# Kernel tuning notes

Measured on AMD Instinct MI355X. Metric: run time of the kernel, lower is better.

Reference implementation:

```python
import jax, jax.numpy as jnp
import numpy as np

T, B, N, KALL, F, ORD, DIN, H, NH, HD, DE, DOUT = 4, 4, 16384, 4, 16384, 3, 4, 64, 4, 16, 4, 64


def setup_inputs() -> dict:
    key = jax.random.key(0)
    ks = jax.random.split(key, 32)
    p = lambda k, shape: (jax.random.normal(k, shape) * 0.1).astype(jnp.float32)
    indices = jax.random.randint(ks[0], (F, ORD), 0, N, dtype=jnp.int32)
    cnt = jnp.zeros((N,), jnp.float32).at[indices.reshape(-1)].add(1.0)
    nnz = jnp.maximum(cnt, 1.0)  # per-node nonzero count (avoid div-by-zero)
    return {
        "h": p(ks[1], (B, N, H)),
        "h_global": p(ks[2], (B, KALL, DOUT)),
        "x": p(ks[3], (T, B, N, DIN)),
        "extra": p(ks[4], (T, B, KALL, DE)),
        "dones": jax.random.bernoulli(ks[5], 0.1, (T, B)),
        "indices": indices,
        "nnz": nnz,
        # GRU cell params (flax GRUCell layout: i-dense with bias, h-dense no bias except n-gate)
        "Wi": p(ks[6], (DIN, 3 * H)), "bi": p(ks[7], (3 * H,)),
        "Wh": p(ks[8], (H, 3 * H)), "bhn": p(ks[9], (H,)),
        # MultiHeadAttention params
        "Wq": p(ks[10], (H, NH, HD)), "bq": p(ks[11], (NH, HD)),
        "Wk": p(ks[12], (H, NH, HD)), "bk": p(ks[13], (NH, HD)),
        "Wv": p(ks[14], (H, NH, HD)), "bv": p(ks[15], (NH, HD)),
        "Wo": p(ks[16], (NH, HD, H)), "bo": p(ks[17], (H,)),
        # output MLP (logit head) and value head
        "W1": p(ks[18], (H + DE, DOUT)), "b1": p(ks[19], (DOUT,)),
        "W2": p(ks[20], (DOUT, 1)), "b2": p(ks[21], (1,)),
        "Wv1": p(ks[22], (H + DE, 1)), "bv1": p(ks[23], (1,)),
    }


def reference(h, h_global, x, extra, dones, indices, nnz,
              Wi, bi, Wh, bhn, Wq, bq, Wk, bk, Wv, bv, Wo, bo,
              W1, b1, W2, b2, Wv1, bv1):
    Hd = Wh.shape[0]

    def gru_step(carry, inp):
        xt, dt = inp  # xt: [B,N,din], dt: [B]
        c = jnp.where(dt[:, None, None], jnp.zeros_like(carry), carry)
        gi = xt @ Wi + bi          # [B,N,3H]
        gh = c @ Wh                # [B,N,3H]
        r = jax.nn.sigmoid(gi[..., :Hd] + gh[..., :Hd])
        z = jax.nn.sigmoid(gi[..., Hd:2 * Hd] + gh[..., Hd:2 * Hd])
        n = jnp.tanh(gi[..., 2 * Hd:] + r * (gh[..., 2 * Hd:] + bhn))
        new = (1.0 - z) * n + z * c
        return new, new

    h_fin, hs = jax.lax.scan(gru_step, h, (x, dones))  # hs: [T,B,N,H]

    # gather per-factor neighbor hidden states
    g = jnp.take(hs, indices, axis=2)  # [T,B,F,ord,H]
    q = jnp.einsum('tbfkh,hnd->tbfknd', g, Wq) + bq
    kk = jnp.einsum('tbfkh,hnd->tbfknd', g, Wk) + bk
    vv = jnp.einsum('tbfkh,hnd->tbfknd', g, Wv) + bv
    scale = 1.0 / np.sqrt(q.shape[-1]).astype(np.float32)
    att = jax.nn.softmax(jnp.einsum('tbfqnd,tbfknd->tbfnqk', q * scale, kk), axis=-1)
    o = jnp.einsum('tbfnqk,tbfknd->tbfqnd', att, vv)
    a = jnp.einsum('tbfknd,ndh->tbfkh', o, Wo) + bo  # [T,B,F,ord,H]

    Tn, Bn = a.shape[0], a.shape[1]
    Nn = nnz.shape[0]
    a_flat = a.reshape(Tn, Bn, -1, a.shape[-1])  # [T,B,F*ord,H]
    # segment-sum scatter back to nodes, normalized by nnz
    y = jnp.zeros((Tn, Bn, Nn, a.shape[-1]), a.dtype).at[:, :, indices.reshape(-1), :].add(a_flat)
    y = y / nnz[None, None, :, None]

    Kall = extra.shape[2]
    N0 = Nn // Kall
    ypi = y.reshape(Tn, Bn, Kall, N0, y.shape[-1])
    y_global = jnp.mean(ypi, axis=3)                       # [T,B,K,H]
    z_global = jnp.concatenate((y_global, extra), axis=3)  # [T,B,K,H+DE]
    extra_t = jnp.broadcast_to(extra[:, :, :, None, :], (Tn, Bn, Kall, N0, extra.shape[-1]))
    z = jnp.concatenate((ypi, extra_t), axis=4).reshape(Tn, Bn, Nn, -1)
    value = (z_global @ Wv1 + bv1).sum(axis=2)             # [T,B,1]
    logit = (jax.nn.relu(z @ W1 + b1) @ W2 + b2).squeeze(axis=3)  # [T,B,N]
    return h_fin, h_global, logit, value.squeeze(axis=-1)
```

## Files before the change

kernel.cpp:

```cpp
#include <hip/hip_runtime.h>
#include <hip/hip_bf16.h>

#define T_ 4
#define B_ 4
#define N_ 16384
#define KALL_ 4
#define F_ 16384
#define ORD_ 3
#define DIN_ 4
#define H_ 64
#define H3_ 192
#define DE_ 4
#define STR 72
#define NE_ 49152

typedef __attribute__((ext_vector_type(8))) short s16x8;
typedef __attribute__((ext_vector_type(4))) float f32x4;
typedef __attribute__((ext_vector_type(2))) float f32x2;
typedef unsigned long long u64;

static __device__ __forceinline__ float b2f(unsigned short u) {
  union { unsigned u; float f; } x; x.u = ((unsigned)u) << 16; return x.f;
}
static __device__ __forceinline__ unsigned short f2b(float f) {
  __hip_bfloat16 h = __float2bfloat16(f);
  union { __hip_bfloat16 h; unsigned short u; } x; x.h = h; return x.u;
}
static __device__ __forceinline__ float sigm_fast(float v) {
  return __builtin_amdgcn_rcpf(1.f + __expf(-v));
}
static __device__ __forceinline__ float tanh_fast(float v) {
  float e = __expf(2.f * v);
  return 1.f - 2.f * __builtin_amdgcn_rcpf(e + 1.f);
}

__global__ __launch_bounds__(256) void k_prep(
    const int* __restrict__ idx, int* __restrict__ cnt,
    const float* __restrict__ Wh, unsigned short* __restrict__ whTg,
    const float* __restrict__ Wq, const float* __restrict__ Wk,
    const float* __restrict__ Wv, const float* __restrict__ Wo,
    unsigned short* __restrict__ wT) {
  const int b = blockIdx.x, tid = threadIdx.x;
  if (b < 192) {
    int e = b * 256 + tid;
    if (e < NE_) atomicAdd(&cnt[idx[e]], 1);
  } else if (b < 240) {
    int i = (b - 192) * 256 + tid;
    int rr = i >> 6, k = i & 63;
    int ct = rr >> 4, c = rr & 15;
    int g = ct >> 2, cg = ct & 3;
    whTg[i] = f2b(Wh[k * H3_ + g * 64 + 4 * c + cg]);
  } else {
    int i = (b - 240) * 256 + tid;
    int m = i >> 12, col = (i >> 6) & 63, k = i & 63;
    const float* Wm = (m == 0) ? Wq : (m == 1) ? Wk : (m == 2) ? Wv : Wo;
    wT[i] = f2b(Wm[k * 64 + col]);
  }
}

__global__ __launch_bounds__(256) void k_csr_scan(
    const int* __restrict__ cnt, int* __restrict__ offs, int* __restrict__ cursor) {
  __shared__ int part[256];
  __shared__ int base[256];
  int t = threadIdx.x;
  int s = 0;
  for (int j = 0; j < 64; ++j) s += cnt[t * 64 + j];
  part[t] = s;
  __syncthreads();
  if (t == 0) {
    int run = 0;
    for (int i = 0; i < 256; ++i) { base[i] = run; run += part[i]; }
  }
  __syncthreads();
  int run = base[t];
  for (int j = 0; j < 64; ++j) {
    offs[t * 64 + j] = run;
    cursor[t * 64 + j] = run;
    run += cnt[t * 64 + j];
  }
  if (t == 255) offs[N_] = run;
}
__global__ __launch_bounds__(256) void k_csr_fill(
    const int* __restrict__ idx, int* __restrict__ cursor, int* __restrict__ elist) {
  int e = blockIdx.x * 256 + threadIdx.x;
  if (e < NE_) {
    int pos = atomicAdd(&cursor[idx[e]], 1);
    elist[pos] = e;
  }
}

__global__ __launch_bounds__(256) void k_gru(
    const float* __restrict__ h0,
    const float* __restrict__ x,
    const int* __restrict__ dones,
    const unsigned short* __restrict__ whTg,
    const float* __restrict__ Wi,
    const float* __restrict__ bi,
    const float* __restrict__ bhn,
    unsigned short* __restrict__ hs,
    float* __restrict__ hfin)
{
  __shared__ __align__(16) short whT[H3_ * 72];
  __shared__ __align__(16) short carry[H_ * 72];
  __shared__ float wiS[5 * H3_];

  const int tid = threadIdx.x;
  const int lane = tid & 63;
  const int w = tid >> 6;
  const int c15 = lane & 15;
  const int hi4 = lane >> 4;
  const int bid = blockIdx.x;
  const int b = bid >> 8;
  const int nbase = (bid & 255) * 64;
  const int hb = 4 * c15;

#pragma unroll
  for (int c = 0; c < 6; ++c) {
    int lin = (c * 256 + tid) * 8;
    int row = lin >> 6, col = lin & 63;
    *(s16x8*)&whT[row * 72 + col] = *(const s16x8*)&whTg[lin];
  }
  for (int i = tid; i < 5 * H3_; i += 256)
    wiS[i] = (i < 4 * H3_) ? Wi[i] : bi[i - 4 * H3_];

  f32x4 cf[4];
#pragma unroll
  for (int r = 0; r < 4; ++r) {
    int row = 16 * w + 4 * hi4 + r;
    cf[r] = *(const f32x4*)&h0[(size_t)(b * N_ + nbase + row) * H_ + hb];
    u64 pk = 0;
#pragma unroll
    for (int e = 0; e < 4; ++e) pk |= (u64)f2b(cf[r][e]) << (16 * e);
    *(u64*)&carry[row * 72 + hb] = pk;
  }

  float bhnr[4];
#pragma unroll
  for (int cg = 0; cg < 4; ++cg) bhnr[cg] = bhn[hb + cg];

  unsigned dmask = 0;
  {
    bool word = true;
#pragma unroll
    for (int i = 0; i < 16; ++i) {
      int v = dones[i];
      if (v != 0 && v != 1 && v != 0x3F800000) word = false;
    }
#pragma unroll
    for (int t = 0; t < T_; ++t) {
      int tb = t * B_ + b;
      bool d = word ? (dones[tb] != 0) : (((const unsigned char*)dones)[tb] != 0);
      if (d) dmask |= (1u << t);
    }
  }

  __syncthreads();

  const int rowA = 16 * w + c15;
  for (int t = 0; t < T_; ++t) {
    if ((dmask >> t) & 1u) {
#pragma unroll
      for (int r = 0; r < 4; ++r) {
        cf[r] = (f32x4){0.f, 0.f, 0.f, 0.f};
        *(u64*)&carry[(16 * w + 4 * hi4 + r) * 72 + hb] = 0ull;
      }
    }

    s16x8 af0 = *(const s16x8*)&carry[rowA * 72 + hi4 * 8];
    s16x8 af1 = *(const s16x8*)&carry[rowA * 72 + 32 + hi4 * 8];

    f32x4 xv[4];
#pragma unroll
    for (int r = 0; r < 4; ++r) {
      const int node = nbase + 16 * w + 4 * hi4 + r;
      xv[r] = *(const f32x4*)&x[(size_t)((t * B_ + b) * N_ + node) * DIN_];
    }

#pragma unroll
    for (int hh = 0; hh < 2; ++hh) {
      f32x4 acc[6];
#pragma unroll
      for (int j = 0; j < 6; ++j) acc[j] = (f32x4){0.f, 0.f, 0.f, 0.f};
#pragma unroll
      for (int j = 0; j < 6; ++j) {
        const int ct = (j >> 1) * 4 + 2 * hh + (j & 1);
        acc[j] = __builtin_amdgcn_mfma_f32_16x16x32_bf16(
            af0, *(const s16x8*)&whT[(16 * ct + c15) * 72 + hi4 * 8], acc[j], 0, 0, 0);
      }
#pragma unroll
      for (int j = 0; j < 6; ++j) {
        const int ct = (j >> 1) * 4 + 2 * hh + (j & 1);
        acc[j] = __builtin_amdgcn_mfma_f32_16x16x32_bf16(
            af1, *(const s16x8*)&whT[(16 * ct + c15) * 72 + 32 + hi4 * 8], acc[j], 0, 0, 0);
      }
      const int hb2 = hb + 2 * hh;
#pragma unroll
      for (int r = 0; r < 4; ++r) {
        f32x2 gi[3];
#pragma unroll
        for (int g = 0; g < 3; ++g) {
          f32x2 s = *(const f32x2*)&wiS[4 * H3_ + g * 64 + hb2];
#pragma unroll
          for (int kk = 0; kk < 4; ++kk) {
            f32x2 wv = *(const f32x2*)&wiS[kk * H3_ + g * 64 + hb2];
            s += xv[r][kk] * wv;
          }
          gi[g] = s;
        }
#pragma unroll
        for (int c2 = 0; c2 < 2; ++c2) {
          const int cg = 2 * hh + c2;
          float rg = sigm_fast(gi[0][c2] + acc[c2][r]);
          float zg = sigm_fast(gi[1][c2] + acc[2 + c2][r]);
          float ng = tanh_fast(gi[2][c2] + rg * (acc[4 + c2][r] + bhnr[cg]));
          float nc = zg * (cf[r][cg] - ng) + ng;
          cf[r][cg] = nc;
        }
      }
    }

#pragma unroll
    for (int r = 0; r < 4; ++r) {
      const int row = 16 * w + 4 * hi4 + r;
      const int node = nbase + row;
      u64 pk = 0;
#pragma unroll
      for (int e = 0; e < 4; ++e) pk |= (u64)f2b(cf[r][e]) << (16 * e);
      *(u64*)&hs[(size_t)((t * B_ + b) * N_ + node) * H_ + hb] = pk;
      *(u64*)&carry[row * 72 + hb] = pk;
      if (t == T_ - 1)
        *(f32x4*)&hfin[(size_t)(b * N_ + node) * H_ + hb] = cf[r];
    }
  }
}

__global__ __launch_bounds__(256) void k_attn(
    const int tb0,
    const unsigned short* __restrict__ hs,
    const int* __restrict__ indices,
    const unsigned short* __restrict__ wT,
    const float* __restrict__ bq, const float* __restrict__ bk,
    const float* __restrict__ bv, const float* __restrict__ bo,
    unsigned short* __restrict__ a_edge)
{
  __shared__ __align__(16) unsigned short bufrag[3072];
  __shared__ __align__(16) float qs[48 * 68];
  __shared__ __align__(16) float ksh[48 * 68];
  __shared__ __align__(8)  unsigned short vs[48 * 68];
  __shared__ int idxs[48];

  const int tid = threadIdx.x;
  const int lane = tid & 63;
  const int w = tid >> 6;
  const int c15 = lane & 15;
  const int hi4 = lane >> 4;
  const int bid = blockIdx.x;
  const int col = 16 * w + c15;
  const int swz = (c15 ^ (hi4 << 2));

  if (tid < 48) idxs[tid] = indices[bid * 48 + tid];

  s16x8 wB[3][2], wB3[2];
#pragma unroll
  for (int m = 0; m < 3; ++m)
#pragma unroll
    for (int ks = 0; ks < 2; ++ks)
      wB[m][ks] = *(const s16x8*)&wT[(m * 64 + col) * 64 + ks * 32 + hi4 * 8];
#pragma unroll
  for (int ks = 0; ks < 2; ++ks)
    wB3[ks] = *(const s16x8*)&wT[(3 * 64 + col) * 64 + ks * 32 + hi4 * 8];
  const float bq_c = bq[col], bk_c = bk[col], bv_c = bv[col], bo_c = bo[col];
  __syncthreads();

  const int grow = tid >> 4, gg = tid & 15;
  const int gks = gg >> 3, gh5 = (gg >> 1) & 3, gj = (gg & 1) * 4;
  size_t goff[3];
  int boff[3];
#pragma unroll
  for (int k = 0; k < 3; ++k) {
    goff[k] = (size_t)idxs[grow + k * 16] * H_ + gg * 4;
    int cr2 = grow ^ (gh5 << 2);
    boff[k] = ((k * 2 + gks) << 9) + ((gh5 * 16 + cr2) << 3) + gj;
  }

  u64 pf[3];
  {
    const unsigned short* hp = hs + (size_t)tb0 * (N_ * H_);
#pragma unroll
    for (int k = 0; k < 3; ++k) pf[k] = *(const u64*)&hp[goff[k]];
  }

  for (int it = 0; it < 8; ++it) {
    __syncthreads();
#pragma unroll
    for (int k = 0; k < 3; ++k) *(u64*)&bufrag[boff[k]] = pf[k];
    __syncthreads();

    s16x8 afr[3][2];
#pragma unroll
    for (int rt = 0; rt < 3; ++rt)
#pragma unroll
      for (int ks = 0; ks < 2; ++ks)
        afr[rt][ks] = *(const s16x8*)&bufrag[((rt * 2 + ks) << 9) + ((hi4 * 16 + swz) << 3)];
#pragma unroll
    for (int rt = 0; rt < 3; ++rt) {
      f32x4 aq = (f32x4){0.f, 0.f, 0.f, 0.f};
      aq = __builtin_amdgcn_mfma_f32_16x16x32_bf16(afr[rt][0], wB[0][0], aq, 0, 0, 0);
      aq = __builtin_amdgcn_mfma_f32_16x16x32_bf16(afr[rt][1], wB[0][1], aq, 0, 0, 0);
#pragma unroll
      for (int r = 0; r < 4; ++r)
        qs[(16 * rt + hi4 * 4 + r) * 68 + col] = (aq[r] + bq_c) * 0.25f;
    }
#pragma unroll
    for (int rt = 0; rt < 3; ++rt) {
      f32x4 ak = (f32x4){0.f, 0.f, 0.f, 0.f};
      ak = __builtin_amdgcn_mfma_f32_16x16x32_bf16(afr[rt][0], wB[1][0], ak, 0, 0, 0);
      ak = __builtin_amdgcn_mfma_f32_16x16x32_bf16(afr[rt][1], wB[1][1], ak, 0, 0, 0);
#pragma unroll
      for (int r = 0; r < 4; ++r)
        ksh[(16 * rt + hi4 * 4 + r) * 68 + col] = ak[r] + bk_c;
    }
#pragma unroll
    for (int rt = 0; rt < 3; ++rt) {
      f32x4 av = (f32x4){0.f, 0.f, 0.f, 0.f};
      av = __builtin_amdgcn_mfma_f32_16x16x32_bf16(afr[rt][0], wB[2][0], av, 0, 0, 0);
      av = __builtin_amdgcn_mfma_f32_16x16x32_bf16(afr[rt][1], wB[2][1], av, 0, 0, 0);
#pragma unroll
      for (int r = 0; r < 4; ++r)
        vs[(16 * rt + hi4 * 4 + r) * 68 + col] = f2b(av[r] + bv_c);
    }
    if (it < 7) {
      const unsigned short* hp = hs + (size_t)(tb0 + it + 1) * (N_ * H_);
#pragma unroll
      for (int k = 0; k < 3; ++k) pf[k] = *(const u64*)&hp[goff[k]];
    }
    __syncthreads();

    {
      int f = tid >> 4, head = (tid >> 2) & 3, dq = tid & 3;
      int colb = head * 16 + dq * 4;
      f32x4 qv[3], kv[3];
      float vv[3][4];
#pragma unroll
      for (int qi = 0; qi < 3; ++qi) {
        int base = (3 * f + qi) * 68 + colb;
        qv[qi] = *(const f32x4*)&qs[base];
        kv[qi] = *(const f32x4*)&ksh[base];
        u64 uv = *(const u64*)&vs[base];
#pragma unroll
        for (int e = 0; e < 4; ++e)
          vv[qi][e] = b2f((unsigned short)(uv >> (16 * e)));
      }
      float s[3][3];
#pragma unroll
      for (int qi = 0; qi < 3; ++qi)
#pragma unroll
        for (int ki = 0; ki < 3; ++ki) {
          float a = qv[qi][0] * kv[ki][0] + qv[qi][1] * kv[ki][1]
                  + qv[qi][2] * kv[ki][2] + qv[qi][3] * kv[ki][3];
          a += __shfl_xor(a, 1, 64);
          a += __shfl_xor(a, 2, 64);
          s[qi][ki] = a;
        }
      const int ks2 = colb >> 5, h5b = (colb >> 3) & 3, jb = colb & 7;
#pragma unroll
      for (int qi = 0; qi < 3; ++qi) {
        float mx = fmaxf(s[qi][0], fmaxf(s[qi][1], s[qi][2]));
        float e0 = __expf(s[qi][0] - mx), e1 = __expf(s[qi][1] - mx), e2 = __expf(s[qi][2] - mx);
        float inv = 1.f / (e0 + e1 + e2);
        e0 *= inv; e1 *= inv; e2 *= inv;
        int row = 3 * f + qi;
        int rt = row >> 4, cr2 = (row & 15) ^ (h5b << 2);
        u64 pack = 0;
#pragma unroll
        for (int e = 0; e < 4; ++e) {
          float o = e0 * vv[0][e] + e1 * vv[1][e] + e2 * vv[2][e];
          pack |= (u64)f2b(o) << (16 * e);
        }
        *(u64*)&bufrag[((rt * 2 + ks2) << 9) + ((h5b * 16 + cr2) << 3) + jb] = pack;
      }
    }
    __syncthreads();

    {
      const size_t abase = (size_t)it * NE_ + (size_t)bid * 48;
#pragma unroll
      for (int rt = 0; rt < 3; ++rt) {
        s16x8 o0 = *(const s16x8*)&bufrag[((rt * 2 + 0) << 9) + ((hi4 * 16 + swz) << 3)];
        s16x8 o1 = *(const s16x8*)&bufrag[((rt * 2 + 1) << 9) + ((hi4 * 16 + swz) << 3)];
        f32x4 acc = (f32x4){0.f, 0.f, 0.f, 0.f};
        acc = __builtin_amdgcn_mfma_f32_16x16x32_bf16(o0, wB3[0], acc, 0, 0, 0);
        acc = __builtin_amdgcn_mfma_f32_16x16x32_bf16(o1, wB3[1], acc, 0, 0, 0);
#pragma unroll
        for (int r = 0; r < 4; ++r) {
          int row = 16 * rt + hi4 * 4 + r;
          a_edge[(abase + row) * H_ + col] = f2b(acc[r] + bo_c);
        }
      }
    }
  }
}

__global__ __launch_bounds__(256) void k_head(
    const int tb0,
    const unsigned short* __restrict__ a_edge,
    const int* __restrict__ offs, const int* __restrict__ elist,
    const float* __restrict__ nnz,
    const float* __restrict__ extra,
    const float* __restrict__ W1, const float* __restrict__ b1,
    const float* __restrict__ W2, const float* __restrict__ b2,
    float* __restrict__ yg,
    float* __restrict__ logit)
{
  __shared__ short w1T[64 * STR];
  __shared__ short arow[64 * STR];
  __shared__ int offsS[65];
  __shared__ int eidS[512];
  __shared__ float hEx[64];
  __shared__ float w2s[64];
  __shared__ float red[4][64];

  const int tid = threadIdx.x;
  const int lane = tid & 63;
  const int w = tid >> 6;
  const int c15 = lane & 15;
  const int hi4 = lane >> 4;
  const int bid = blockIdx.x;
  const int ls = bid >> 8;
  const int tb = tb0 + ls;
  const int nbase = (bid & 255) * 64;
  const int kall = nbase >> 12;

  for (int i = tid; i < 4096; i += 256) {
    int k = i >> 6, colc = i & 63;
    w1T[colc * STR + k] = (short)f2b(W1[i]);
  }
  if (tid < 65) offsS[tid] = offs[nbase + tid];
  if (tid < 64) {
    float s = b1[tid];
#pragma unroll
    for (int e = 0; e < 4; ++e)
      s += extra[(tb * KALL_ + kall) * DE_ + e] * W1[(64 + e) * 64 + tid];
    hEx[tid] = s;
    w2s[tid] = W2[tid];
  }
  const int ebeg = offs[nbase];
  const int ecnt = offs[nbase + 64] - ebeg;
  const bool fast = (ecnt <= 512);
  if (tid == 0) eidS[0] = 0;
  if (fast) {
    for (int j = tid; j < ecnt; j += 256) eidS[j] = elist[ebeg + j];
  }
  __syncthreads();

  const size_t ebase = (size_t)ls * NE_;
  float accp = 0.f;
  if (fast) {
    for (int r = w; r < 64; r += 4) {
      const int beg = offsS[r] - ebeg, end = offsS[r + 1] - ebeg;
      float s = 0.f;
#pragma unroll
      for (int u = 0; u < 8; ++u) {
        int p = beg + u;
        bool valid = p < end;
        int pc = valid ? p : 0;
        float v = b2f(a_edge[(ebase + eidS[pc]) * H_ + lane]);
        s += valid ? v : 0.f;
      }
      for (int p = beg + 8; p < end; ++p)
        s += b2f(a_edge[(ebase + eidS[p]) * H_ + lane]);
      float val = s / fmaxf((float)(end - beg), 1.f);
      accp += val;
      arow[r * STR + lane] = (short)f2b(val);
    }
  } else {
    for (int r = w; r < 64; r += 4) {
      const int beg = offsS[r], end = offsS[r + 1];
      float s = 0.f;
      for (int p = beg; p < end; ++p)
        s += b2f(a_edge[(ebase + elist[p]) * H_ + lane]);
      float val = s / fmaxf((float)(end - beg), 1.f);
      accp += val;
      arow[r * STR + lane] = (short)f2b(val);
    }
  }
  red[w][lane] = accp;
  __syncthreads();

  f32x4 acc[4];
#pragma unroll
  for (int ct = 0; ct < 4; ++ct) acc[ct] = (f32x4){0.f, 0.f, 0.f, 0.f};
#pragma unroll
  for (int ks = 0; ks < 2; ++ks) {
    int kb = ks * 32 + hi4 * 8;
    s16x8 af = *(const s16x8*)&arow[(16 * w + c15) * STR + kb];
#pragma unroll
    for (int ct = 0; ct < 4; ++ct) {
      s16x8 bfr = *(const s16x8*)&w1T[(16 * ct + c15) * STR + kb];
      acc[ct] = __builtin_amdgcn_mfma_f32_16x16x32_bf16(af, bfr, acc[ct], 0, 0, 0);
    }
  }
  const float b2v = b2[0];
#pragma unroll
  for (int r = 0; r < 4; ++r) {
    float s = 0.f;
#pragma unroll
    for (int ct = 0; ct < 4; ++ct) {
      int colc = 16 * ct + c15;
      s += fmaxf(acc[ct][r] + hEx[colc], 0.f) * w2s[colc];
    }
    s += __shfl_xor(s, 1, 64);
    s += __shfl_xor(s, 2, 64);
    s += __shfl_xor(s, 4, 64);
    s += __shfl_xor(s, 8, 64);
    if (c15 == 0)
      logit[tb * N_ + nbase + 16 * w + hi4 * 4 + r] = s + b2v;
  }
  if (tid < 64) {
    float sv = red[0][tid] + red[1][tid] + red[2][tid] + red[3][tid];
    atomicAdd(&yg[(tb * KALL_ + kall) * H_ + tid], sv);
  }
}

__global__ __launch_bounds__(256) void k_final(
    const float* __restrict__ yg,
    const float* __restrict__ extra,
    const float* __restrict__ Wv1, const float* __restrict__ bv1,
    const float* __restrict__ hg_in,
    float* __restrict__ value_out,
    float* __restrict__ hg_out)
{
  const int tid = threadIdx.x;
  if (tid < 16) {
    const float bv = bv1[0];
    float v = 0.f;
    for (int kall = 0; kall < 4; ++kall) {
      float s = bv;
      for (int hh = 0; hh < 64; ++hh)
        s += (yg[(tid * KALL_ + kall) * H_ + hh] * (1.f / 4096.f)) * Wv1[hh];
      for (int e = 0; e < 4; ++e)
        s += extra[(tid * KALL_ + kall) * DE_ + e] * Wv1[64 + e];
      v += s;
    }
    value_out[tid] = v;
  }
  for (int i = tid; i < 1024; i += 256) hg_out[i] = hg_in[i];
}

extern "C" void kernel_launch(void* const* d_in, const int* in_sizes, int n_in,
                              void* d_out, int out_size, void* d_ws, size_t ws_size,
                              hipStream_t stream)
{
  (void)in_sizes; (void)n_in; (void)out_size; (void)ws_size;
  const float* h0    = (const float*)d_in[0];
  const float* hg    = (const float*)d_in[1];
  const float* x     = (const float*)d_in[2];
  const float* extra = (const float*)d_in[3];
  const int*   dn    = (const int*)d_in[4];
  const int*   idx   = (const int*)d_in[5];
  const float* nnz   = (const float*)d_in[6];
  const float* Wi    = (const float*)d_in[7];
  const float* bi    = (const float*)d_in[8];
  const float* Wh    = (const float*)d_in[9];
  const float* bhn   = (const float*)d_in[10];
  const float* Wq    = (const float*)d_in[11];
  const float* bq    = (const float*)d_in[12];
  const float* Wk    = (const float*)d_in[13];
  const float* bk    = (const float*)d_in[14];
  const float* Wv    = (const float*)d_in[15];
  const float* bv    = (const float*)d_in[16];
  const float* Wo    = (const float*)d_in[17];
  const float* bo    = (const float*)d_in[18];
  const float* W1    = (const float*)d_in[19];
  const float* b1    = (const float*)d_in[20];
  const float* W2    = (const float*)d_in[21];
  const float* b2    = (const float*)d_in[22];
  const float* Wv1   = (const float*)d_in[23];
  const float* bv1   = (const float*)d_in[24];

  float* out = (float*)d_out;
  float* out_hfin  = out;
  float* out_hg    = out + 4194304;
  float* out_logit = out + 4195328;
  float* out_value = out + 4457472;

  char* wsb = (char*)d_ws;
  float*          yg     = (float*)wsb;
  int*            cnt    = (int*)(wsb + 16384);
  int*            offs   = (int*)(wsb + 81920);
  int*            cursor = (int*)(wsb + 147584);
  int*            elist  = (int*)(wsb + 213120);
  unsigned short* whTg   = (unsigned short*)(wsb + 409728);
  unsigned short* wT     = (unsigned short*)(wsb + 434304);
  unsigned short* hs     = (unsigned short*)(wsb + 524288);
  unsigned short* a_edge = (unsigned short*)(wsb + 34078720);

  hipMemsetAsync(wsb, 0, 81920, stream);
  k_prep<<<304, 256, 0, stream>>>(idx, cnt, Wh, whTg, Wq, Wk, Wv, Wo, wT);
  k_csr_scan<<<1, 256, 0, stream>>>(cnt, offs, cursor);
  k_csr_fill<<<192, 256, 0, stream>>>(idx, cursor, elist);
  k_gru<<<1024, 256, 0, stream>>>(h0, x, dn, whTg, Wi, bi, bhn, hs, out_hfin);
  for (int half = 0; half < 2; ++half) {
    const int tb0 = half * 8;
    k_attn<<<1024, 256, 0, stream>>>(tb0, hs, idx, wT, bq, bk, bv, bo, a_edge);
    k_head<<<2048, 256, 0, stream>>>(tb0, a_edge, offs, elist, nnz, extra,
                                     W1, b1, W2, b2, yg, out_logit);
  }
  k_final<<<1, 256, 0, stream>>>(yg, extra, Wv1, bv1, hg, out_value, out_hg);
}
```

Measured before the change: 334.3 us.

## Apply attention output projection per node after segment mean instead of per edge

```diff
diff --git a/kernel.cpp b/kernel.cpp
--- a/kernel.cpp
+++ b/kernel.cpp
@@ -157,6 +157,7 @@
   __syncthreads();
 
   const int rowA = 16 * w + c15;
+#pragma unroll 1
   for (int t = 0; t < T_; ++t) {
     if ((dmask >> t) & 1u) {
 #pragma unroll
@@ -240,7 +241,7 @@
     const int* __restrict__ indices,
     const unsigned short* __restrict__ wT,
     const float* __restrict__ bq, const float* __restrict__ bk,
-    const float* __restrict__ bv, const float* __restrict__ bo,
+    const float* __restrict__ bv,
     unsigned short* __restrict__ a_edge)
 {
   __shared__ __align__(16) unsigned short bufrag[3072];
@@ -260,16 +261,13 @@
 
   if (tid < 48) idxs[tid] = indices[bid * 48 + tid];
 
-  s16x8 wB[3][2], wB3[2];
+  s16x8 wB[3][2];
 #pragma unroll
   for (int m = 0; m < 3; ++m)
 #pragma unroll
     for (int ks = 0; ks < 2; ++ks)
       wB[m][ks] = *(const s16x8*)&wT[(m * 64 + col) * 64 + ks * 32 + hi4 * 8];
-#pragma unroll
-  for (int ks = 0; ks < 2; ++ks)
-    wB3[ks] = *(const s16x8*)&wT[(3 * 64 + col) * 64 + ks * 32 + hi4 * 8];
-  const float bq_c = bq[col], bk_c = bk[col], bv_c = bv[col], bo_c = bo[col];
+  const float bq_c = bq[col], bk_c = bk[col], bv_c = bv[col];
   __syncthreads();
 
   const int grow = tid >> 4, gg = tid & 15;
@@ -291,7 +289,6 @@
   }
 
   for (int it = 0; it < 8; ++it) {
-    __syncthreads();
 #pragma unroll
     for (int k = 0; k < 3; ++k) *(u64*)&bufrag[boff[k]] = pf[k];
     __syncthreads();
@@ -362,7 +359,7 @@
           a += __shfl_xor(a, 2, 64);
           s[qi][ki] = a;
         }
-      const int ks2 = colb >> 5, h5b = (colb >> 3) & 3, jb = colb & 7;
+      const size_t abase = (size_t)it * NE_ + (size_t)bid * 48;
 #pragma unroll
       for (int qi = 0; qi < 3; ++qi) {
         float mx = fmaxf(s[qi][0], fmaxf(s[qi][1], s[qi][2]));
@@ -370,34 +367,16 @@
         float inv = 1.f / (e0 + e1 + e2);
         e0 *= inv; e1 *= inv; e2 *= inv;
         int row = 3 * f + qi;
-        int rt = row >> 4, cr2 = (row & 15) ^ (h5b << 2);
         u64 pack = 0;
 #pragma unroll
         for (int e = 0; e < 4; ++e) {
           float o = e0 * vv[0][e] + e1 * vv[1][e] + e2 * vv[2][e];
           pack |= (u64)f2b(o) << (16 * e);
         }
-        *(u64*)&bufrag[((rt * 2 + ks2) << 9) + ((h5b * 16 + cr2) << 3) + jb] = pack;
+        *(u64*)&a_edge[(abase + row) * H_ + colb] = pack;
       }
     }
     __syncthreads();
-
-    {
-      const size_t abase = (size_t)it * NE_ + (size_t)bid * 48;
-#pragma unroll
-      for (int rt = 0; rt < 3; ++rt) {
-        s16x8 o0 = *(const s16x8*)&bufrag[((rt * 2 + 0) << 9) + ((hi4 * 16 + swz) << 3)];
-        s16x8 o1 = *(const s16x8*)&bufrag[((rt * 2 + 1) << 9) + ((hi4 * 16 + swz) << 3)];
-        f32x4 acc = (f32x4){0.f, 0.f, 0.f, 0.f};
-        acc = __builtin_amdgcn_mfma_f32_16x16x32_bf16(o0, wB3[0], acc, 0, 0, 0);
-        acc = __builtin_amdgcn_mfma_f32_16x16x32_bf16(o1, wB3[1], acc, 0, 0, 0);
-#pragma unroll
-        for (int r = 0; r < 4; ++r) {
-          int row = 16 * rt + hi4 * 4 + r;
-          a_edge[(abase + row) * H_ + col] = f2b(acc[r] + bo_c);
-        }
-      }
-    }
   }
 }
 
@@ -405,7 +384,8 @@
     const int tb0,
     const unsigned short* __restrict__ a_edge,
     const int* __restrict__ offs, const int* __restrict__ elist,
-    const float* __restrict__ nnz,
+    const unsigned short* __restrict__ wT,
+    const float* __restrict__ bo,
     const float* __restrict__ extra,
     const float* __restrict__ W1, const float* __restrict__ b1,
     const float* __restrict__ W2, const float* __restrict__ b2,
@@ -418,6 +398,7 @@
   __shared__ int eidS[512];
   __shared__ float hEx[64];
   __shared__ float w2s[64];
+  __shared__ float hasES[64];
   __shared__ float red[4][64];
 
   const int tid = threadIdx.x;
@@ -444,6 +425,15 @@
     hEx[tid] = s;
     w2s[tid] = W2[tid];
   }
+  s16x8 wo_b[2][4];
+  float boc[4];
+#pragma unroll
+  for (int ct = 0; ct < 4; ++ct) {
+    boc[ct] = bo[16 * ct + c15];
+#pragma unroll
+    for (int ks = 0; ks < 2; ++ks)
+      wo_b[ks][ct] = *(const s16x8*)&wT[(192 + 16 * ct + c15) * 64 + ks * 32 + hi4 * 8];
+  }
   const int ebeg = offs[nbase];
   const int ecnt = offs[nbase + 64] - ebeg;
   const bool fast = (ecnt <= 512);
@@ -454,7 +444,6 @@
   __syncthreads();
 
   const size_t ebase = (size_t)ls * NE_;
-  float accp = 0.f;
   if (fast) {
     for (int r = w; r < 64; r += 4) {
       const int beg = offsS[r] - ebeg, end = offsS[r + 1] - ebeg;
@@ -470,8 +459,8 @@
       for (int p = beg + 8; p < end; ++p)
         s += b2f(a_edge[(ebase + eidS[p]) * H_ + lane]);
       float val = s / fmaxf((float)(end - beg), 1.f);
-      accp += val;
       arow[r * STR + lane] = (short)f2b(val);
+      if (lane == 0) hasES[r] = (end > beg) ? 1.f : 0.f;
     }
   } else {
     for (int r = w; r < 64; r += 4) {
@@ -480,12 +469,44 @@
       for (int p = beg; p < end; ++p)
         s += b2f(a_edge[(ebase + elist[p]) * H_ + lane]);
       float val = s / fmaxf((float)(end - beg), 1.f);
-      accp += val;
       arow[r * STR + lane] = (short)f2b(val);
-    }
-  }
-  red[w][lane] = accp;
+      if (lane == 0) hasES[r] = (end > beg) ? 1.f : 0.f;
+    }
+  }
   __syncthreads();
+
+  f32x4 acco[4];
+#pragma unroll
+  for (int ct = 0; ct < 4; ++ct) acco[ct] = (f32x4){0.f, 0.f, 0.f, 0.f};
+#pragma unroll
+  for (int ks = 0; ks < 2; ++ks) {
+    int kb = ks * 32 + hi4 * 8;
+    s16x8 af = *(const s16x8*)&arow[(16 * w + c15) * STR + kb];
+#pragma unroll
+    for (int ct = 0; ct < 4; ++ct)
+      acco[ct] = __builtin_amdgcn_mfma_f32_16x16x32_bf16(af, wo_b[ks][ct], acco[ct], 0, 0, 0);
+  }
+  float sumy[4] = {0.f, 0.f, 0.f, 0.f};
+#pragma unroll
+  for (int r = 0; r < 4; ++r) {
+    const int rowr = 16 * w + hi4 * 4 + r;
+    const float hase = hasES[rowr];
+#pragma unroll
+    for (int ct = 0; ct < 4; ++ct) {
+      float y = acco[ct][r] + hase * boc[ct];
+      arow[rowr * STR + 16 * ct + c15] = (short)f2b(y);
+      sumy[ct] += y;
+    }
+  }
+#pragma unroll
+  for (int ct = 0; ct < 4; ++ct) {
+    sumy[ct] += __shfl_xor(sumy[ct], 16, 64);
+    sumy[ct] += __shfl_xor(sumy[ct], 32, 64);
+  }
+  if (hi4 == 0) {
+#pragma unroll
+    for (int ct = 0; ct < 4; ++ct) red[w][16 * ct + c15] = sumy[ct];
+  }
 
   f32x4 acc[4];
 #pragma unroll
@@ -516,6 +537,7 @@
     if (c15 == 0)
       logit[tb * N_ + nbase + 16 * w + hi4 * 4 + r] = s + b2v;
   }
+  __syncthreads();
   if (tid < 64) {
     float sv = red[0][tid] + red[1][tid] + red[2][tid] + red[3][tid];
     atomicAdd(&yg[(tb * KALL_ + kall) * H_ + tid], sv);
@@ -577,6 +599,7 @@
   const float* b2    = (const float*)d_in[22];
   const float* Wv1   = (const float*)d_in[23];
   const float* bv1   = (const float*)d_in[24];
+  (void)nnz;
 
   float* out = (float*)d_out;
   float* out_hfin  = out;
@@ -602,8 +625,8 @@
   k_gru<<<1024, 256, 0, stream>>>(h0, x, dn, whTg, Wi, bi, bhn, hs, out_hfin);
   for (int half = 0; half < 2; ++half) {
     const int tb0 = half * 8;
-    k_attn<<<1024, 256, 0, stream>>>(tb0, hs, idx, wT, bq, bk, bv, bo, a_edge);
-    k_head<<<2048, 256, 0, stream>>>(tb0, a_edge, offs, elist, nnz, extra,
+    k_attn<<<1024, 256, 0, stream>>>(tb0, hs, idx, wT, bq, bk, bv, a_edge);
+    k_head<<<2048, 256, 0, stream>>>(tb0, a_edge, offs, elist, wT, bo, extra,
                                      W1, b1, W2, b2, yg, out_logit);
   }
   k_final<<<1, 256, 0, stream>>>(yg, extra, Wv1, bv1, hg, out_value, out_hg);
```

After: 332.3 us. About the same (-0.6%).
